# Optimization experiments

Hardware: AMD Instinct MI355X
Metric: run time of the kernel (lower is better)

## Reference

```python
import jax, jax.numpy as jnp
import numpy as np

SCALE = 100.0  # scale_up in logsumexp_pool


def setup_inputs() -> dict:
    key = jax.random.key(0)
    # NHWC, channels_last
    x = jax.random.normal(key, (8, 256, 256, 64), dtype=jnp.float32)
    return {"x": x}


def reference(x):
    # Faithful to logsumexp_pool: transpose NHWC -> [C,H,W,N], scale by 100,
    # extract 2x2 stride-2 VALID patches (depth axis = 2*2*N after transpose,
    # so the logsumexp reduces over the window AND the batch dim), descale,
    # expand_dims + transpose -> output [1, H/2, W/2, C].
    N, H, W, C = x.shape
    t = jnp.transpose(x, (3, 1, 2, 0)) * SCALE          # [C, H, W, N]
    # stride 2, kernel 2, VALID padding, even H/W -> non-overlapping windows;
    t = t.reshape(C, H // 2, 2, W // 2, 2, N)
    r = jax.nn.logsumexp(t, axis=(2, 4, 5)) * (1.0 / SCALE)  # [C, H/2, W/2]
    return jnp.transpose(r[..., None], (3, 1, 2, 0))    # [1, H/2, W/2, C]
```

## Files before the change

### kernel.cpp

```cpp
#include <hip/hip_runtime.h>


constexpr float SCALE = 100.0f;
constexpr float INV_SCALE = 0.01f;

__global__ __launch_bounds__(256) void lse_pool_kernel(const float* __restrict__ x,
                                                       float* __restrict__ out) {
    const int t   = blockIdx.x * 256 + threadIdx.x;
    const int cg  = t & 15;
    const int pix = t >> 4;
    const int wo  = pix & 127;
    const int ho  = pix >> 7;
    const int c   = cg << 2;
    const int h0  = ho << 1;
    const int w0  = wo << 1;

    float4 vals[32];
    int i = 0;
#pragma unroll
    for (int n = 0; n < 8; ++n) {
#pragma unroll
        for (int dh = 0; dh < 2; ++dh) {
#pragma unroll
            for (int dw = 0; dw < 2; ++dw) {
                const size_t off =
                    ((((size_t)n * 256 + (size_t)(h0 + dh)) * 256) + (size_t)(w0 + dw)) * 64
                    + (size_t)c;
                vals[i++] = *reinterpret_cast<const float4*>(x + off);
            }
        }
    }

    float4 m = vals[0];
#pragma unroll
    for (int k = 1; k < 32; ++k) {
        m.x = fmaxf(m.x, vals[k].x);
        m.y = fmaxf(m.y, vals[k].y);
        m.z = fmaxf(m.z, vals[k].z);
        m.w = fmaxf(m.w, vals[k].w);
    }

    float4 s = make_float4(0.f, 0.f, 0.f, 0.f);
#pragma unroll
    for (int k = 0; k < 32; ++k) {
        s.x += __expf((vals[k].x - m.x) * SCALE);
        s.y += __expf((vals[k].y - m.y) * SCALE);
        s.z += __expf((vals[k].z - m.z) * SCALE);
        s.w += __expf((vals[k].w - m.w) * SCALE);
    }

    float4 r;
    r.x = m.x + __logf(s.x) * INV_SCALE;
    r.y = m.y + __logf(s.y) * INV_SCALE;
    r.z = m.z + __logf(s.z) * INV_SCALE;
    r.w = m.w + __logf(s.w) * INV_SCALE;

    *reinterpret_cast<float4*>(out + (size_t)pix * 64 + (size_t)c) = r;
}

extern "C" void kernel_launch(void* const* d_in, const int* in_sizes, int n_in,
                              void* d_out, int out_size, void* d_ws, size_t ws_size,
                              hipStream_t stream) {
    const float* x = (const float*)d_in[0];
    float* out = (float*)d_out;
    lse_pool_kernel<<<1024, 256, 0, stream>>>(x, out);
}
```

Baseline: 187.5 us.

## Remap threads to contiguous input rows and use online logsumexp with shuffle merge

Each wavefront now reads contiguous 1KB input row segments (8 input pixels × 64 channels), so loads are fully coalesced. The old mapping had each thread gather 32 strided float4s. An online max/sum merge replaces holding 32 float4 registers, which lowers register pressure. Horizontal window pairs are combined with a cross-lane shuffle, and half the lanes write outputs. In exchange the kernel does more exp evaluations per element because of the rescaling in the online merge.

New measurement: 185.6 us. About the same (-1.0%).

```diff
diff --git a/kernel.cpp b/kernel.cpp
--- a/kernel.cpp
+++ b/kernel.cpp
@@ -4,58 +4,82 @@
 constexpr float SCALE = 100.0f;
 constexpr float INV_SCALE = 0.01f;
 
+__device__ inline void chunk_merge(const float4& v0, const float4& v1,
+                                   float m[4], float s[4]) {
+    const float e0[4] = {v0.x, v0.y, v0.z, v0.w};
+    const float e1[4] = {v1.x, v1.y, v1.z, v1.w};
+#pragma unroll
+    for (int j = 0; j < 4; ++j) {
+        const float cm = fmaxf(e0[j], e1[j]);
+        const float cs = __expf((e0[j] - cm) * SCALE) + __expf((e1[j] - cm) * SCALE);
+        const float mn = fmaxf(m[j], cm);
+        s[j] = s[j] * __expf((m[j] - mn) * SCALE) + cs * __expf((cm - mn) * SCALE);
+        m[j] = mn;
+    }
+}
+
 __global__ __launch_bounds__(256) void lse_pool_kernel(const float* __restrict__ x,
                                                        float* __restrict__ out) {
-    const int t   = blockIdx.x * 256 + threadIdx.x;
-    const int cg  = t & 15;
-    const int pix = t >> 4;
-    const int wo  = pix & 127;
-    const int ho  = pix >> 7;
-    const int c   = cg << 2;
-    const int h0  = ho << 1;
-    const int w0  = wo << 1;
+    const int tid = blockIdx.x * 256 + threadIdx.x;
+    const int l   = tid & 63;
+    const int wv  = tid >> 6;
+    const int ho  = wv >> 5;
+    const int p0  = (wv & 31) << 3;
 
-    float4 vals[32];
-    int i = 0;
+    const size_t NS = (size_t)256 * 256 * 64;
+    const size_t HS = (size_t)256 * 64;
+    const float* base = x + (((size_t)(2 * ho) * 256) + (size_t)p0) * 64 + (size_t)(l * 4);
+
+    float mA[4], sA[4], mB[4], sB[4];
 #pragma unroll
+    for (int j = 0; j < 4; ++j) { mA[j] = -1e30f; sA[j] = 0.f; mB[j] = -1e30f; sB[j] = 0.f; }
+
+#pragma unroll 2
     for (int n = 0; n < 8; ++n) {
+        const float* pn = base + (size_t)n * NS;
+        const float4 a0 = *reinterpret_cast<const float4*>(pn);
+        const float4 b0 = *reinterpret_cast<const float4*>(pn + 256);
+        const float4 a1 = *reinterpret_cast<const float4*>(pn + HS);
+        const float4 b1 = *reinterpret_cast<const float4*>(pn + HS + 256);
+        chunk_merge(a0, a1, mA, sA);
+        chunk_merge(b0, b1, mB, sB);
+    }
+
 #pragma unroll
-        for (int dh = 0; dh < 2; ++dh) {
-#pragma unroll
-            for (int dw = 0; dw < 2; ++dw) {
-                const size_t off =
-                    ((((size_t)n * 256 + (size_t)(h0 + dh)) * 256) + (size_t)(w0 + dw)) * 64
-                    + (size_t)c;
-                vals[i++] = *reinterpret_cast<const float4*>(x + off);
-            }
+    for (int j = 0; j < 4; ++j) {
+        {
+            const float m2 = __shfl_xor(mA[j], 16);
+            const float s2 = __shfl_xor(sA[j], 16);
+            const float mn = fmaxf(mA[j], m2);
+            sA[j] = sA[j] * __expf((mA[j] - mn) * SCALE) + s2 * __expf((m2 - mn) * SCALE);
+            mA[j] = mn;
+        }
+        {
+            const float m2 = __shfl_xor(mB[j], 16);
+            const float s2 = __shfl_xor(sB[j], 16);
+            const float mn = fmaxf(mB[j], m2);
+            sB[j] = sB[j] * __expf((mB[j] - mn) * SCALE) + s2 * __expf((m2 - mn) * SCALE);
+            mB[j] = mn;
         }
     }
 
-    float4 m = vals[0];
-#pragma unroll
-    for (int k = 1; k < 32; ++k) {
-        m.x = fmaxf(m.x, vals[k].x);
-        m.y = fmaxf(m.y, vals[k].y);
-        m.z = fmaxf(m.z, vals[k].z);
-        m.w = fmaxf(m.w, vals[k].w);
+    if ((l & 16) == 0) {
+        float4 rA, rB;
+        rA.x = mA[0] + __logf(sA[0]) * INV_SCALE;
+        rA.y = mA[1] + __logf(sA[1]) * INV_SCALE;
+        rA.z = mA[2] + __logf(sA[2]) * INV_SCALE;
+        rA.w = mA[3] + __logf(sA[3]) * INV_SCALE;
+        rB.x = mB[0] + __logf(sB[0]) * INV_SCALE;
+        rB.y = mB[1] + __logf(sB[1]) * INV_SCALE;
+        rB.z = mB[2] + __logf(sB[2]) * INV_SCALE;
+        rB.w = mB[3] + __logf(sB[3]) * INV_SCALE;
+
+        const int c  = (l & 15) << 2;
+        const int wo = (p0 >> 1) + (l >> 5);
+        const size_t o = ((size_t)ho * 128 + (size_t)wo) * 64 + (size_t)c;
+        *reinterpret_cast<float4*>(out + o)            = rA;
+        *reinterpret_cast<float4*>(out + o + 2 * 64)   = rB;
     }
-
-    float4 s = make_float4(0.f, 0.f, 0.f, 0.f);
-#pragma unroll
-    for (int k = 0; k < 32; ++k) {
-        s.x += __expf((vals[k].x - m.x) * SCALE);
-        s.y += __expf((vals[k].y - m.y) * SCALE);
-        s.z += __expf((vals[k].z - m.z) * SCALE);
-        s.w += __expf((vals[k].w - m.w) * SCALE);
-    }
-
-    float4 r;
-    r.x = m.x + __logf(s.x) * INV_SCALE;
-    r.y = m.y + __logf(s.y) * INV_SCALE;
-    r.z = m.z + __logf(s.z) * INV_SCALE;
-    r.w = m.w + __logf(s.w) * INV_SCALE;
-
-    *reinterpret_cast<float4*>(out + (size_t)pix * 64 + (size_t)c) = r;
 }
 
 extern "C" void kernel_launch(void* const* d_in, const int* in_sizes, int n_in,
```
